# Optimization experiments

Measured on AMD Instinct MI355X. Metric: run time of the kernel, lower is better.

Reference implementation:

```python
import jax, jax.numpy as jnp
import numpy as np

TAU = 0.7
N_NODES = 1024
N_EDGES = 32768

def _mlp3(x, W1, b1, W2, b2, W3, b3):
    h = jax.nn.relu(x @ W1 + b1)
    h = jax.nn.relu(h @ W2 + b2)
    return h @ W3 + b3

def _gcn_conv(x, src, dst, W, b, n):
    # PyG GCNConv(add_self_loops=False): out = D^-1/2 A D^-1/2 (x W) + b
    deg = jax.ops.segment_sum(jnp.ones(src.shape[0], x.dtype), dst, num_segments=n)
    dinv = jnp.where(deg > 0, jax.lax.rsqrt(jnp.maximum(deg, 1.0)), 0.0)
    h = x @ W
    msg = h[src] * (dinv[src] * dinv[dst])[:, None]
    return jax.ops.segment_sum(msg, dst, num_segments=n) + b

def _forward(x1, x11, x2, mlp_W1, mlp_b1, mlp_W2, mlp_b2, mlp_W3, mlp_b3,
             m1_W1, m1_b1, m1_W2, m1_b2, m1_W3, m1_b3,
             wm1, bp1, bp2, wm12, wm13, class2,
             gcn1_W, gcn1_b, wm2, gcn2_W, gcn2_b, fc_W, fc_b, src, dst):
    n = x1.shape[0]
    logits = _mlp3(x1, mlp_W1, mlp_b1, mlp_W2, mlp_b2, mlp_W3, mlp_b3)  # [N,3]
    g = _mlp3(x11, m1_W1, m1_b1, m1_W2, m1_b2, m1_W3, m1_b3)            # [N,2]
    # hard argmax routing, softened: tau at argmax, (1-tau)/2 at the 2 others
    oh = jax.nn.one_hot(jnp.argmax(logits, axis=1), 3, dtype=logits.dtype)
    r = oh * TAU + (1.0 - oh) * ((1.0 - TAU) * 0.5)                     # [N,3]
    # fused form of: (einsum('nj,jkl',g,class2) * x2[...,None]).sum(-1) + g@b1
    res1 = jnp.einsum('nj,jkl,nk->nk', g, class2, x2) + g @ bp1         # [N,768]
    # fused form of: (einsum('nj,jkl',r,wm1) * res1[...,None]).sum(-1) + r@b2
    res1 = jnp.einsum('nj,jkl,nk->nk', r, wm1, res1) + r @ bp2          # [N,768]
    h1 = jax.nn.relu(_gcn_conv(res1, src, dst, gcn1_W, gcn1_b, n))      # [N,256]
    h1 = (r @ wm12) * h1 + 2e-4 * (res1 @ wm13)                         # [N,256]
    res2 = jnp.einsum('nj,jkl,nk->nk', r, wm2, h1)                      # [N,256]
    h2 = jax.nn.relu(_gcn_conv(res2, src, dst, gcn2_W, gcn2_b, n))      # [N,32]
    return jax.nn.log_softmax(h2 @ fc_W + fc_b, axis=1)                 # [N,8]

def setup_inputs():
    key = jax.random.key(0)
    ks = jax.random.split(key, 32)
    f = jnp.float32
    nrm = lambda i, s, sc=0.05: sc * jax.random.normal(ks[i], s, f)
    return {
        'x1': nrm(0, (N_NODES, 768), 1.0),
        'x11': nrm(1, (N_NODES, 768), 1.0),
        'x2': nrm(2, (N_NODES, 768), 1.0),
        'mlp_W1': nrm(3, (768, 512)), 'mlp_b1': jnp.zeros((512,), f),
        'mlp_W2': nrm(4, (512, 512)), 'mlp_b2': jnp.zeros((512,), f),
        'mlp_W3': nrm(5, (512, 3)), 'mlp_b3': jnp.zeros((3,), f),
        'm1_W1': nrm(6, (768, 512)), 'm1_b1': jnp.zeros((512,), f),
        'm1_W2': nrm(7, (512, 512)), 'm1_b2': jnp.zeros((512,), f),
        'm1_W3': nrm(8, (512, 2)), 'm1_b3': jnp.zeros((2,), f),
        'wm1': nrm(9, (3, 768, 256)),
        'bp1': jnp.zeros((2, 768), f),
        'bp2': jnp.zeros((3, 768), f),
        'wm12': jnp.ones((3, 256), f),
        'wm13': nrm(10, (768, 256)),
        'class2': jnp.ones((2, 768, 64), f),
        'gcn1_W': nrm(11, (768, 256)), 'gcn1_b': jnp.zeros((256,), f),
        'wm2': nrm(12, (3, 256, 256)),
        'gcn2_W': nrm(13, (256, 32)), 'gcn2_b': jnp.zeros((32,), f),
        'fc_W': nrm(14, (32, 8)), 'fc_b': jnp.zeros((8,), f),
        'edge_index': jax.random.randint(ks[15], (2, N_EDGES), 0, N_NODES),
    }

def reference(x1, x11, x2, mlp_W1, mlp_b1, mlp_W2, mlp_b2, mlp_W3, mlp_b3,
              m1_W1, m1_b1, m1_W2, m1_b2, m1_W3, m1_b3,
              wm1, bp1, bp2, wm12, wm13, class2,
              gcn1_W, gcn1_b, wm2, gcn2_W, gcn2_b, fc_W, fc_b, edge_index):
    src, dst = edge_index[0], edge_index[1]
    return _forward(x1, x11, x2, mlp_W1, mlp_b1, mlp_W2, mlp_b2, mlp_W3, mlp_b3,
                    m1_W1, m1_b1, m1_W2, m1_b2, m1_W3, m1_b3,
                    wm1, bp1, bp2, wm12, wm13, class2,
                    gcn1_W, gcn1_b, wm2, gcn2_W, gcn2_b, fc_W, fc_b, src, dst)
```

## Files before the change

kernel.cpp:

```cpp
#include <hip/hip_runtime.h>
#include <hip/hip_bf16.h>

#define NN 1024
#define NE 32768
#define TAU 0.7f
#define GAPT 0.01f

typedef __attribute__((ext_vector_type(8))) short short8;
typedef __attribute__((ext_vector_type(4))) float f32x4;

__device__ inline ushort bf16rne(float x) {
    union { float f; unsigned u; } a; a.f = x;
    unsigned r = (a.u + 0x7FFFu + ((a.u >> 16) & 1u)) >> 16;
    return (ushort)r;
}
__device__ inline float bf16tof(ushort h) {
    union { unsigned u; float f; } a; a.u = ((unsigned)h) << 16;
    return a.f;
}
__device__ inline void bf16split(float x, ushort& h, ushort& l) {
    h = bf16rne(x);
    l = bf16rne(x - bf16tof(h));
}

template <int K, int EPI>
__device__ __forceinline__ void gemm_wave(
    int lane, int rt, int ct,
    const ushort* __restrict__ Ah, const ushort* __restrict__ Al,
    const ushort* __restrict__ Bh, const ushort* __restrict__ Bl,
    const float* __restrict__ bias, const float* __restrict__ W3,
    float* __restrict__ Cf, ushort* __restrict__ Oh, ushort* __restrict__ Ol, int N) {
    int r0 = rt * 16, c0 = ct * 32;
    int g = lane >> 4, q = lane & 15;
    const ushort* pah = Ah + (size_t)(r0 + q) * K + g * 8;
    const ushort* pal = Al + (size_t)(r0 + q) * K + g * 8;
    const ushort* pb0h = Bh + (size_t)(c0 + q) * K + g * 8;
    const ushort* pb0l = Bl + (size_t)(c0 + q) * K + g * 8;
    const ushort* pb1h = pb0h + (size_t)16 * K;
    const ushort* pb1l = pb0l + (size_t)16 * K;
    f32x4 acc0 = {0.f, 0.f, 0.f, 0.f};
    f32x4 acc1 = {0.f, 0.f, 0.f, 0.f};
#pragma unroll 2
    for (int k0 = 0; k0 < K; k0 += 32) {
        short8 ah = *(const short8*)(pah + k0);
        short8 al = *(const short8*)(pal + k0);
        short8 b0h = *(const short8*)(pb0h + k0);
        short8 b0l = *(const short8*)(pb0l + k0);
        short8 b1h = *(const short8*)(pb1h + k0);
        short8 b1l = *(const short8*)(pb1l + k0);
        acc0 = __builtin_amdgcn_mfma_f32_16x16x32_bf16(ah, b0h, acc0, 0, 0, 0);
        acc1 = __builtin_amdgcn_mfma_f32_16x16x32_bf16(ah, b1h, acc1, 0, 0, 0);
        acc0 = __builtin_amdgcn_mfma_f32_16x16x32_bf16(ah, b0l, acc0, 0, 0, 0);
        acc1 = __builtin_amdgcn_mfma_f32_16x16x32_bf16(ah, b1l, acc1, 0, 0, 0);
        acc0 = __builtin_amdgcn_mfma_f32_16x16x32_bf16(al, b0h, acc0, 0, 0, 0);
        acc1 = __builtin_amdgcn_mfma_f32_16x16x32_bf16(al, b1h, acc1, 0, 0, 0);
    }
    int col0 = c0 + q, col1 = c0 + 16 + q;
    if constexpr (EPI == 0) {
#pragma unroll
        for (int i = 0; i < 4; i++) {
            int row = r0 + g * 4 + i;
            Cf[(size_t)row * N + col0] = acc0[i];
            Cf[(size_t)row * N + col1] = acc1[i];
        }
    } else if constexpr (EPI == 1) {
        float bv0 = bias[col0], bv1 = bias[col1];
#pragma unroll
        for (int i = 0; i < 4; i++) {
            int row = r0 + g * 4 + i;
            float a0 = fmaxf(acc0[i] + bv0, 0.f);
            float a1 = fmaxf(acc1[i] + bv1, 0.f);
            ushort h, l;
            bf16split(a0, h, l);
            Oh[(size_t)row * N + col0] = h;
            Ol[(size_t)row * N + col0] = l;
            bf16split(a1, h, l);
            Oh[(size_t)row * N + col1] = h;
            Ol[(size_t)row * N + col1] = l;
        }
    } else {
        constexpr int J = (EPI == 2) ? 3 : 2;
        constexpr int STR = (EPI == 2) ? 4 : 2;
        float bv0 = bias[col0], bv1 = bias[col1];
        float s[4][J];
#pragma unroll
        for (int i = 0; i < 4; i++) {
            float a0 = fmaxf(acc0[i] + bv0, 0.f);
            float a1 = fmaxf(acc1[i] + bv1, 0.f);
#pragma unroll
            for (int j = 0; j < J; j++)
                s[i][j] = a0 * W3[col0 * J + j] + a1 * W3[col1 * J + j];
        }
#pragma unroll
        for (int i = 0; i < 4; i++)
#pragma unroll
            for (int j = 0; j < J; j++) {
                float v = s[i][j];
#pragma unroll
                for (int m = 1; m < 16; m <<= 1) v += __shfl_xor(v, m);
                s[i][j] = v;
            }
        if (q == 0) {
#pragma unroll
            for (int i = 0; i < 4; i++) {
                int row = r0 + g * 4 + i;
#pragma unroll
                for (int j = 0; j < J; j++) atomicAdd(&Cf[(size_t)row * STR + j], s[i][j]);
            }
        }
    }
}

template <int M, int N, int K, int EPI>
__global__ __launch_bounds__(256) void gemm3(
    const ushort* __restrict__ Ah, const ushort* __restrict__ Al,
    const ushort* __restrict__ Bh, const ushort* __restrict__ Bl,
    float* __restrict__ Cf) {
    constexpr int RT = M / 16;
    constexpr int JOBS = RT * (N / 32);
    int wid = (blockIdx.x * 256 + threadIdx.x) >> 6;
    if (wid >= JOBS) return;
    gemm_wave<K, EPI>(threadIdx.x & 63, wid % RT, wid / RT, Ah, Al, Bh, Bl,
                      nullptr, nullptr, Cf, nullptr, nullptr, N);
}

template <int K, int EPI0, int EPI1, bool FILL>
__global__ __launch_bounds__(256) void gemm_pair(
    const ushort* __restrict__ Ah0, const ushort* __restrict__ Al0,
    const ushort* __restrict__ Bh0, const ushort* __restrict__ Bl0,
    const float* __restrict__ bias0, const float* __restrict__ W30,
    float* __restrict__ Cf0, ushort* __restrict__ Oh0, ushort* __restrict__ Ol0,
    const ushort* __restrict__ Ah1, const ushort* __restrict__ Al1,
    const ushort* __restrict__ Bh1, const ushort* __restrict__ Bl1,
    const float* __restrict__ bias1, const float* __restrict__ W31,
    float* __restrict__ Cf1, ushort* __restrict__ Oh1, ushort* __restrict__ Ol1,
    const int* __restrict__ esrc, const int* __restrict__ edst,
    int* __restrict__ cursor, int* __restrict__ adj) {
    if (FILL && blockIdx.x >= 512) {
        int e = (blockIdx.x - 512) * 256 + threadIdx.x;
        int d = edst[e];
        int slot = atomicAdd(&cursor[d], 1);
        adj[slot] = esrc[e];
        return;
    }
    int wid = (blockIdx.x * 256 + threadIdx.x) >> 6;
    int lane = threadIdx.x & 63;
    int pair = wid >> 10;
    int widl = wid & 1023;
    int rt = widl & 63, ct = widl >> 6;
    if (pair == 0)
        gemm_wave<K, EPI0>(lane, rt, ct, Ah0, Al0, Bh0, Bl0, bias0, W30, Cf0, Oh0, Ol0, 512);
    else
        gemm_wave<K, EPI1>(lane, rt, ct, Ah1, Al1, Bh1, Bl1, bias1, W31, Cf1, Oh1, Ol1, 512);
}

__device__ void dev_zero(int sub, int t, float* zbase) {
    for (int i = sub * 256 + t; i < 6144; i += 512) zbase[i] = 0.f;
}

__device__ void dev_tabs(int sub, int t, const float* class2, const float* wm1,
                         const float* wm2, float* C2s, float* Wm1s, float* Wm2s) {
    int i = sub * 256 + t;
    if (i < 1536) {
        const float* p = class2 + (size_t)i * 64;
        float s = 0.f;
        for (int l = 0; l < 64; l++) s += p[l];
        C2s[i] = s;
    } else if (i < 3840) {
        int j = i - 1536;
        const float* p = wm1 + (size_t)j * 256;
        float s = 0.f;
        for (int l = 0; l < 256; l++) s += p[l];
        Wm1s[j] = s;
    } else if (i < 4608) {
        int j = i - 3840;
        const float* p = wm2 + (size_t)j * 256;
        float s = 0.f;
        for (int l = 0; l < 256; l++) s += p[l];
        Wm2s[j] = s;
    }
}

__device__ void dev_splitx(int sub, int t, const float* __restrict__ X,
                           ushort* __restrict__ Xh, ushort* __restrict__ Xl) {
    int j = sub * 256 + t;
    float4 v = ((const float4*)X)[j];
    ushort h0, l0, h1, l1, h2, l2, h3, l3;
    bf16split(v.x, h0, l0);
    bf16split(v.y, h1, l1);
    bf16split(v.z, h2, l2);
    bf16split(v.w, h3, l3);
    ((ushort4*)Xh)[j] = make_ushort4(h0, h1, h2, h3);
    ((ushort4*)Xl)[j] = make_ushort4(l0, l1, l2, l3);
}

__device__ void dev_csr(int t, const int* __restrict__ edst, int* __restrict__ rowst,
                        int* __restrict__ cursor, float* __restrict__ dinv) {
    __shared__ int s[NN];
    s[t] = 0;
    __syncthreads();
    for (int j = 0; j < 32; j++) atomicAdd(&s[edst[j * 1024 + t]], 1);
    __syncthreads();
    int d = s[t];
    dinv[t] = d > 0 ? rsqrtf((float)d) : 0.f;
    __syncthreads();
    for (int off = 1; off < NN; off <<= 1) {
        int v = (t >= off) ? s[t - off] : 0;
        __syncthreads();
        s[t] += v;
        __syncthreads();
    }
    rowst[t + 1] = s[t];
    if (t == 0) rowst[0] = 0;
    cursor[t] = s[t] - d;
}

__global__ __launch_bounds__(1024) void aux0(
    const float* class2, const float* wm1, const float* wm2,
    float* C2s, float* Wm1s, float* Wm2s, float* zbase,
    const float* x1, ushort* XH1, ushort* XL1,
    const float* x11, ushort* XH2, ushort* XL2,
    const float* W1a, ushort* W1AH, ushort* W1AL,
    const float* W1b, ushort* W1BH, ushort* W1BL,
    const float* W2a, ushort* W2AH, ushort* W2AL,
    const float* W2b, ushort* W2BH, ushort* W2BL,
    const float* G1W, ushort* GWH, ushort* GWL,
    const float* W13, const float* G2W, ushort* G2TH, ushort* G2TL,
    const int* edst, int* rowst, int* cursor, float* dinv) {
    if (blockIdx.x == 807) {
        dev_csr(threadIdx.x, edst, rowst, cursor, dinv);
        return;
    }
    __shared__ float tb[4][32][33];
    int quad = threadIdx.x >> 8;
    int t = threadIdx.x & 255;
    int sub = blockIdx.x * 4 + quad;
    const float* W = nullptr;
    ushort *Th = nullptr, *Tl = nullptr;
    int K = 0, N = 0, tile = 0;
    if (sub >= 3220)      { W = G2W; Th = G2TH; Tl = G2TL; K = 256; N = 32;  tile = sub - 3220; }
    else if (sub >= 3028) { W = W13; Th = GWH + 256 * 768; Tl = GWL + 256 * 768; K = 768; N = 256; tile = sub - 3028; }
    else if (sub >= 2836) { W = G1W; Th = GWH; Tl = GWL; K = 768; N = 256; tile = sub - 2836; }
    else if (sub >= 2580) { W = W2b; Th = W2BH; Tl = W2BL; K = 512; N = 512; tile = sub - 2580; }
    else if (sub >= 2324) { W = W2a; Th = W2AH; Tl = W2AL; K = 512; N = 512; tile = sub - 2324; }
    else if (sub >= 1940) { W = W1b; Th = W1BH; Tl = W1BL; K = 768; N = 512; tile = sub - 1940; }
    else if (sub >= 1556) { W = W1a; Th = W1AH; Tl = W1AL; K = 768; N = 512; tile = sub - 1556; }
    int k0 = 0, n0 = 0;
    if (W) {
        k0 = (tile % (K / 32)) * 32;
        n0 = (tile / (K / 32)) * 32;
        int tx = t % 32, ty = t / 32;
        for (int i = ty; i < 32; i += 8)
            tb[quad][i][tx] = W[(size_t)(k0 + i) * N + n0 + tx];
    } else if (sub < 2) dev_zero(sub, t, zbase);
    else if (sub < 20) dev_tabs(sub - 2, t, class2, wm1, wm2, C2s, Wm1s, Wm2s);
    else if (sub < 788) dev_splitx(sub - 20, t, x1, XH1, XL1);
    else dev_splitx(sub - 788, t, x11, XH2, XL2);
    __syncthreads();
    if (W) {
        int tx = t % 32, ty = t / 32;
        for (int i = ty; i < 32; i += 8) {
            float v = tb[quad][tx][i];
            ushort h, l;
            bf16split(v, h, l);
            Th[(size_t)(n0 + i) * K + k0 + tx] = h;
            Tl[(size_t)(n0 + i) * K + k0 + tx] = l;
        }
    }
}

__global__ __launch_bounds__(256) void finrep(
    const float* __restrict__ LG, const float* __restrict__ b3, float* __restrict__ rbuf,
    const float* __restrict__ x1, const float* __restrict__ W1, const float* __restrict__ b1,
    const float* __restrict__ W2, const float* __restrict__ b2, const float* __restrict__ W3) {
    __shared__ int snode[4];
    __shared__ int scnt;
    __shared__ float part[4][512];
    __shared__ float xs[768];
    __shared__ float h1[512];
    __shared__ float h2[512];
    int t = threadIdx.x;
    if (t == 0) scnt = 0;
    __syncthreads();
    if (t < 4) {
        int n = blockIdx.x * 4 + t;
        float l0 = LG[n * 4 + 0] + b3[0];
        float l1 = LG[n * 4 + 1] + b3[1];
        float l2 = LG[n * 4 + 2] + b3[2];
        int am = 0;
        float mv = l0;
        if (l1 > mv) { mv = l1; am = 1; }
        if (l2 > mv) { mv = l2; am = 2; }
        float sec = (am == 0) ? fmaxf(l1, l2) : ((am == 1) ? fmaxf(l0, l2) : fmaxf(l0, l1));
        float lo = (1.f - TAU) * 0.5f;
        rbuf[n * 4 + 0] = (am == 0) ? TAU : lo;
        rbuf[n * 4 + 1] = (am == 1) ? TAU : lo;
        rbuf[n * 4 + 2] = (am == 2) ? TAU : lo;
        if (mv - sec < GAPT) {
            int s = atomicAdd(&scnt, 1);
            snode[s] = n;
        }
    }
    __syncthreads();
    int cnt = scnt;
    int w = t >> 6, l = t & 63;
    for (int it = 0; it < cnt; it++) {
        int n = snode[it];
        for (int k = t; k < 768; k += 256) xs[k] = x1[(size_t)n * 768 + k];
        __syncthreads();
        {
            float acc[8] = {0.f, 0.f, 0.f, 0.f, 0.f, 0.f, 0.f, 0.f};
            for (int k = w * 192; k < (w + 1) * 192; k++) {
                float xv = xs[k];
                const float* wr = W1 + (size_t)k * 512 + l;
#pragma unroll
                for (int c = 0; c < 8; c++) acc[c] += xv * wr[64 * c];
            }
#pragma unroll
            for (int c = 0; c < 8; c++) part[w][l + 64 * c] = acc[c];
        }
        __syncthreads();
        for (int d = t; d < 512; d += 256)
            h1[d] = fmaxf(part[0][d] + part[1][d] + part[2][d] + part[3][d] + b1[d], 0.f);
        __syncthreads();
        {
            float acc[8] = {0.f, 0.f, 0.f, 0.f, 0.f, 0.f, 0.f, 0.f};
            for (int k = w * 128; k < (w + 1) * 128; k++) {
                float xv = h1[k];
                const float* wr = W2 + (size_t)k * 512 + l;
#pragma unroll
                for (int c = 0; c < 8; c++) acc[c] += xv * wr[64 * c];
            }
#pragma unroll
            for (int c = 0; c < 8; c++) part[w][l + 64 * c] = acc[c];
        }
        __syncthreads();
        for (int d = t; d < 512; d += 256)
            h2[d] = fmaxf(part[0][d] + part[1][d] + part[2][d] + part[3][d] + b2[d], 0.f);
        __syncthreads();
        if (t < 64) {
            float p0 = 0.f, p1 = 0.f, p2 = 0.f;
            for (int k = t; k < 512; k += 64) {
                float hv = h2[k];
                p0 += hv * W3[k * 3 + 0];
                p1 += hv * W3[k * 3 + 1];
                p2 += hv * W3[k * 3 + 2];
            }
            for (int off = 32; off; off >>= 1) {
                p0 += __shfl_down(p0, off);
                p1 += __shfl_down(p1, off);
                p2 += __shfl_down(p2, off);
            }
            if (t == 0) {
                float l0 = p0 + b3[0], l1 = p1 + b3[1], l2 = p2 + b3[2];
                int am = 0;
                float mv = l0;
                if (l1 > mv) { mv = l1; am = 1; }
                if (l2 > mv) { mv = l2; am = 2; }
                float lo = (1.f - TAU) * 0.5f;
                rbuf[n * 4 + 0] = (am == 0) ? TAU : lo;
                rbuf[n * 4 + 1] = (am == 1) ? TAU : lo;
                rbuf[n * 4 + 2] = (am == 2) ? TAU : lo;
            }
        }
        __syncthreads();
    }
}

__global__ __launch_bounds__(256) void res1_kernel(
    const float* __restrict__ x2, const float* __restrict__ G, const float* __restrict__ m1b3,
    const float* __restrict__ rbuf, const float* __restrict__ C2s, const float* __restrict__ bp1,
    const float* __restrict__ Wm1s, const float* __restrict__ bp2,
    ushort* __restrict__ r1h, ushort* __restrict__ r1l) {
    int idx = blockIdx.x * 256 + threadIdx.x;
    int n = idx / 192;
    int kq = (idx % 192) * 4;
    float g0 = G[n * 2 + 0] + m1b3[0], g1 = G[n * 2 + 1] + m1b3[1];
    float r0 = rbuf[n * 4 + 0], r1 = rbuf[n * 4 + 1], r2 = rbuf[n * 4 + 2];
    float4 xv = *(const float4*)(x2 + (size_t)n * 768 + kq);
    float4 c0 = *(const float4*)(C2s + kq);
    float4 c1 = *(const float4*)(C2s + 768 + kq);
    float4 p0 = *(const float4*)(bp1 + kq);
    float4 p1 = *(const float4*)(bp1 + 768 + kq);
    float4 w0 = *(const float4*)(Wm1s + kq);
    float4 w1 = *(const float4*)(Wm1s + 768 + kq);
    float4 w2 = *(const float4*)(Wm1s + 1536 + kq);
    float4 q0 = *(const float4*)(bp2 + kq);
    float4 q1 = *(const float4*)(bp2 + 768 + kq);
    float4 q2 = *(const float4*)(bp2 + 1536 + kq);
    float o[4];
    o[0] = (xv.x * (g0 * c0.x + g1 * c1.x) + g0 * p0.x + g1 * p1.x) * (r0 * w0.x + r1 * w1.x + r2 * w2.x) + r0 * q0.x + r1 * q1.x + r2 * q2.x;
    o[1] = (xv.y * (g0 * c0.y + g1 * c1.y) + g0 * p0.y + g1 * p1.y) * (r0 * w0.y + r1 * w1.y + r2 * w2.y) + r0 * q0.y + r1 * q1.y + r2 * q2.y;
    o[2] = (xv.z * (g0 * c0.z + g1 * c1.z) + g0 * p0.z + g1 * p1.z) * (r0 * w0.z + r1 * w1.z + r2 * w2.z) + r0 * q0.z + r1 * q1.z + r2 * q2.z;
    o[3] = (xv.w * (g0 * c0.w + g1 * c1.w) + g0 * p0.w + g1 * p1.w) * (r0 * w0.w + r1 * w1.w + r2 * w2.w) + r0 * q0.w + r1 * q1.w + r2 * q2.w;
    ushort h[4], l[4];
#pragma unroll
    for (int i = 0; i < 4; i++) bf16split(o[i], h[i], l[i]);
    size_t off = ((size_t)n * 768 + kq) / 4;
    ((ushort4*)r1h)[off] = make_ushort4(h[0], h[1], h[2], h[3]);
    ((ushort4*)r1l)[off] = make_ushort4(l[0], l[1], l[2], l[3]);
}

__global__ __launch_bounds__(256) void gather1_combine(
    const float* __restrict__ gcw, const int* __restrict__ rowst, const int* __restrict__ adj,
    const float* __restrict__ dinv, const float* __restrict__ gcn1_b,
    const float* __restrict__ rbuf, const float* __restrict__ wm12,
    const float* __restrict__ Wm2s, ushort* __restrict__ res2h, ushort* __restrict__ res2l) {
    int n = blockIdx.x;
    int k = threadIdx.x;
    int lane = threadIdx.x & 63;
    int e0 = rowst[n], e1 = rowst[n + 1];
    float acc = 0.f;
    for (int base = e0; base < e1; base += 64) {
        int idx = base + lane;
        int s_i = 0;
        float w_i = 0.f;
        if (idx < e1) { s_i = adj[idx]; w_i = dinv[s_i]; }
        int mm = min(64, e1 - base);
        for (int j = 0; j < mm; j++) {
            int s = __shfl(s_i, j);
            float w = __shfl(w_i, j);
            acc += gcw[(size_t)s * 512 + k] * w;
        }
    }
    float h1 = dinv[n] * acc + gcn1_b[k];
    float mv = gcw[(size_t)n * 512 + 256 + k];
    float r0 = rbuf[n * 4 + 0], r1 = rbuf[n * 4 + 1], r2 = rbuf[n * 4 + 2];
    float a = r0 * wm12[k] + r1 * wm12[256 + k] + r2 * wm12[512 + k];
    float w = r0 * Wm2s[k] + r1 * Wm2s[256 + k] + r2 * Wm2s[512 + k];
    float v = w * (a * fmaxf(h1, 0.f) + 2e-4f * mv);
    ushort h, l;
    bf16split(v, h, l);
    res2h[(size_t)n * 256 + k] = h;
    res2l[(size_t)n * 256 + k] = l;
}

__global__ __launch_bounds__(64) void gather2_fc(
    const float* __restrict__ g2h, const int* __restrict__ rowst, const int* __restrict__ adj,
    const float* __restrict__ dinv, const float* __restrict__ gcn2_b,
    const float* __restrict__ fcW, const float* __restrict__ fcb, float* __restrict__ out) {
    __shared__ float h2s[2][32];
    int t = threadIdx.x;
    int half = t >> 5, k = t & 31;
    int n = blockIdx.x * 2 + half;
    int e0 = rowst[n], e1 = rowst[n + 1];
    float acc = 0.f;
    for (int base = e0; base < e1; base += 32) {
        int idx = base + k;
        int s_i = 0;
        float w_i = 0.f;
        if (idx < e1) { s_i = adj[idx]; w_i = dinv[s_i]; }
        int mm = min(32, e1 - base);
        for (int j = 0; j < mm; j++) {
            int s = __shfl(s_i, j, 32);
            float w = __shfl(w_i, j, 32);
            acc += g2h[(size_t)s * 32 + k] * w;
        }
    }
    h2s[half][k] = fmaxf(dinv[n] * acc + gcn2_b[k], 0.f);
    __syncthreads();
    if (t < 16) {
        int nn = t >> 3, j = t & 7;
        const float* hr = h2s[nn];
        float logit = fcb[j];
#pragma unroll
        for (int i = 0; i < 32; i++) logit += hr[i] * fcW[i * 8 + j];
        float m = logit;
        for (int off = 4; off; off >>= 1) m = fmaxf(m, __shfl_xor(m, off, 8));
        float e = expf(logit - m), s = e;
        for (int off = 4; off; off >>= 1) s += __shfl_xor(s, off, 8);
        out[(size_t)(blockIdx.x * 2 + nn) * 8 + j] = logit - m - logf(s);
    }
}

extern "C" void kernel_launch(void* const* d_in, const int* in_sizes, int n_in,
                              void* d_out, int out_size, void* d_ws, size_t ws_size,
                              hipStream_t stream) {
    const float* x1     = (const float*)d_in[0];
    const float* x11    = (const float*)d_in[1];
    const float* x2     = (const float*)d_in[2];
    const float* mlp_W1 = (const float*)d_in[3];
    const float* mlp_b1 = (const float*)d_in[4];
    const float* mlp_W2 = (const float*)d_in[5];
    const float* mlp_b2 = (const float*)d_in[6];
    const float* mlp_W3 = (const float*)d_in[7];
    const float* mlp_b3 = (const float*)d_in[8];
    const float* m1_W1  = (const float*)d_in[9];
    const float* m1_b1  = (const float*)d_in[10];
    const float* m1_W2  = (const float*)d_in[11];
    const float* m1_b2  = (const float*)d_in[12];
    const float* m1_W3  = (const float*)d_in[13];
    const float* m1_b3  = (const float*)d_in[14];
    const float* wm1    = (const float*)d_in[15];
    const float* bp1    = (const float*)d_in[16];
    const float* bp2    = (const float*)d_in[17];
    const float* wm12   = (const float*)d_in[18];
    const float* wm13   = (const float*)d_in[19];
    const float* class2 = (const float*)d_in[20];
    const float* gcn1_W = (const float*)d_in[21];
    const float* gcn1_b = (const float*)d_in[22];
    const float* wm2    = (const float*)d_in[23];
    const float* gcn2_W = (const float*)d_in[24];
    const float* gcn2_b = (const float*)d_in[25];
    const float* fc_W   = (const float*)d_in[26];
    const float* fc_b   = (const float*)d_in[27];
    const int* eidx     = (const int*)d_in[28];
    const int* esrc = eidx;
    const int* edst = eidx + NE;

    char* ws = (char*)d_ws;
    ushort* XH1   = (ushort*)(ws + 0x0000000);
    ushort* XL1   = (ushort*)(ws + 0x0180000);
    ushort* XH2   = (ushort*)(ws + 0x0300000);
    ushort* XL2   = (ushort*)(ws + 0x0480000);
    ushort* W1AH  = (ushort*)(ws + 0x0600000);
    ushort* W1AL  = (ushort*)(ws + 0x06C0000);
    ushort* W1BH  = (ushort*)(ws + 0x0780000);
    ushort* W1BL  = (ushort*)(ws + 0x0840000);
    ushort* W2AH  = (ushort*)(ws + 0x0900000);
    ushort* W2AL  = (ushort*)(ws + 0x0980000);
    ushort* W2BH  = (ushort*)(ws + 0x0A00000);
    ushort* W2BL  = (ushort*)(ws + 0x0A80000);
    ushort* GWH   = (ushort*)(ws + 0x0B00000);
    ushort* GWL   = (ushort*)(ws + 0x0BC0000);
    ushort* G2TH  = (ushort*)(ws + 0x0C80000);
    ushort* G2TL  = (ushort*)(ws + 0x0C84000);
    ushort* HS1AH = (ushort*)(ws + 0x0D00000);
    ushort* HS1AL = (ushort*)(ws + 0x0E00000);
    ushort* HS1BH = (ushort*)(ws + 0x0F00000);
    ushort* HS1BL = (ushort*)(ws + 0x1000000);
    ushort* RES1H = (ushort*)(ws + 0x1100000);
    ushort* RES1L = (ushort*)(ws + 0x1280000);
    float*  GCW   = (float*)(ws + 0x1400000);
    ushort* RES2H = (ushort*)(ws + 0x1600000);
    ushort* RES2L = (ushort*)(ws + 0x1680000);
    float*  G2H   = (float*)(ws + 0x1700000);
    float* LOGITS = (float*)(ws + 0x1740000);
    float* GBUF   = (float*)(ws + 0x1744000);
    float* RBUF   = (float*)(ws + 0x1746000);
    float* DINV   = (float*)(ws + 0x174A000);
    int*   ROWST  = (int*)(ws + 0x174B000);
    int*   CURS   = (int*)(ws + 0x174D000);
    int*   ADJ    = (int*)(ws + 0x174E000);
    float* C2S    = (float*)(ws + 0x1770000);
    float* WM1S   = (float*)(ws + 0x1772000);
    float* WM2S   = (float*)(ws + 0x1775000);

    aux0<<<808, 1024, 0, stream>>>(class2, wm1, wm2, C2S, WM1S, WM2S, LOGITS,
                                   x1, XH1, XL1, x11, XH2, XL2,
                                   mlp_W1, W1AH, W1AL, m1_W1, W1BH, W1BL,
                                   mlp_W2, W2AH, W2AL, m1_W2, W2BH, W2BL,
                                   gcn1_W, GWH, GWL, wm13, gcn2_W, G2TH, G2TL,
                                   edst, ROWST, CURS, DINV);
    gemm_pair<768, 1, 1, true><<<640, 256, 0, stream>>>(
        XH1, XL1, W1AH, W1AL, mlp_b1, nullptr, nullptr, HS1AH, HS1AL,
        XH2, XL2, W1BH, W1BL, m1_b1, nullptr, nullptr, HS1BH, HS1BL,
        esrc, edst, CURS, ADJ);
    gemm_pair<512, 2, 3, false><<<512, 256, 0, stream>>>(
        HS1AH, HS1AL, W2AH, W2AL, mlp_b2, mlp_W3, LOGITS, nullptr, nullptr,
        HS1BH, HS1BL, W2BH, W2BL, m1_b2, m1_W3, GBUF, nullptr, nullptr,
        nullptr, nullptr, nullptr, nullptr);
    finrep<<<256, 256, 0, stream>>>(LOGITS, mlp_b3, RBUF, x1, mlp_W1, mlp_b1,
                                    mlp_W2, mlp_b2, mlp_W3);
    res1_kernel<<<768, 256, 0, stream>>>(x2, GBUF, m1_b3, RBUF, C2S, bp1, WM1S, bp2,
                                         RES1H, RES1L);
    gemm3<1024, 512, 768, 0><<<256, 256, 0, stream>>>(RES1H, RES1L, GWH, GWL, GCW);
    gather1_combine<<<NN, 256, 0, stream>>>(GCW, ROWST, ADJ, DINV, gcn1_b, RBUF,
                                            wm12, WM2S, RES2H, RES2L);
    gemm3<1024, 32, 256, 0><<<16, 256, 0, stream>>>(RES2H, RES2L, G2TH, G2TL, G2H);
    gather2_fc<<<NN / 2, 64, 0, stream>>>(G2H, ROWST, ADJ, DINV, gcn2_b, fc_W, fc_b,
                                          (float*)d_out);
}
```

Baseline: 193.3 us.

## Split CSR build across kernels: parallel degree count, scan rider, fill rider

```diff
diff --git a/kernel.cpp b/kernel.cpp
--- a/kernel.cpp
+++ b/kernel.cpp
@@ -124,7 +124,7 @@
                       nullptr, nullptr, Cf, nullptr, nullptr, N);
 }
 
-template <int K, int EPI0, int EPI1, bool FILL>
+template <int K, int EPI0, int EPI1, int RIDER>
 __global__ __launch_bounds__(256) void gemm_pair(
     const ushort* __restrict__ Ah0, const ushort* __restrict__ Al0,
     const ushort* __restrict__ Bh0, const ushort* __restrict__ Bl0,
@@ -135,8 +135,39 @@
     const float* __restrict__ bias1, const float* __restrict__ W31,
     float* __restrict__ Cf1, ushort* __restrict__ Oh1, ushort* __restrict__ Ol1,
     const int* __restrict__ esrc, const int* __restrict__ edst,
-    int* __restrict__ cursor, int* __restrict__ adj) {
-    if (FILL && blockIdx.x >= 512) {
+    const int* __restrict__ deg, int* __restrict__ rowst, int* __restrict__ cursor,
+    float* __restrict__ dinv, int* __restrict__ adj) {
+    if (RIDER == 1 && blockIdx.x >= 512) {
+        __shared__ int ps[256];
+        int t = threadIdx.x;
+        int4 d4 = *(const int4*)(deg + t * 4);
+        int sum = d4.x + d4.y + d4.z + d4.w;
+        ps[t] = sum;
+        __syncthreads();
+        for (int off = 1; off < 256; off <<= 1) {
+            int v = (t >= off) ? ps[t - off] : 0;
+            __syncthreads();
+            ps[t] += v;
+            __syncthreads();
+        }
+        int r0 = ps[t] - sum;
+        int r1 = r0 + d4.x, r2 = r1 + d4.y, r3 = r2 + d4.z;
+        rowst[t * 4 + 0] = r0;
+        rowst[t * 4 + 1] = r1;
+        rowst[t * 4 + 2] = r2;
+        rowst[t * 4 + 3] = r3;
+        if (t == 255) rowst[1024] = r3 + d4.w;
+        cursor[t * 4 + 0] = r0;
+        cursor[t * 4 + 1] = r1;
+        cursor[t * 4 + 2] = r2;
+        cursor[t * 4 + 3] = r3;
+        dinv[t * 4 + 0] = d4.x > 0 ? rsqrtf((float)d4.x) : 0.f;
+        dinv[t * 4 + 1] = d4.y > 0 ? rsqrtf((float)d4.y) : 0.f;
+        dinv[t * 4 + 2] = d4.z > 0 ? rsqrtf((float)d4.z) : 0.f;
+        dinv[t * 4 + 3] = d4.w > 0 ? rsqrtf((float)d4.w) : 0.f;
+        return;
+    }
+    if (RIDER == 2 && blockIdx.x >= 512) {
         int e = (blockIdx.x - 512) * 256 + threadIdx.x;
         int d = edst[e];
         int slot = atomicAdd(&cursor[d], 1);
@@ -194,27 +225,6 @@
     ((ushort4*)Xl)[j] = make_ushort4(l0, l1, l2, l3);
 }
 
-__device__ void dev_csr(int t, const int* __restrict__ edst, int* __restrict__ rowst,
-                        int* __restrict__ cursor, float* __restrict__ dinv) {
-    __shared__ int s[NN];
-    s[t] = 0;
-    __syncthreads();
-    for (int j = 0; j < 32; j++) atomicAdd(&s[edst[j * 1024 + t]], 1);
-    __syncthreads();
-    int d = s[t];
-    dinv[t] = d > 0 ? rsqrtf((float)d) : 0.f;
-    __syncthreads();
-    for (int off = 1; off < NN; off <<= 1) {
-        int v = (t >= off) ? s[t - off] : 0;
-        __syncthreads();
-        s[t] += v;
-        __syncthreads();
-    }
-    rowst[t + 1] = s[t];
-    if (t == 0) rowst[0] = 0;
-    cursor[t] = s[t] - d;
-}
-
 __global__ __launch_bounds__(1024) void aux0(
     const float* class2, const float* wm1, const float* wm2,
     float* C2s, float* Wm1s, float* Wm2s, float* zbase,
@@ -226,11 +236,7 @@
     const float* W2b, ushort* W2BH, ushort* W2BL,
     const float* G1W, ushort* GWH, ushort* GWL,
     const float* W13, const float* G2W, ushort* G2TH, ushort* G2TL,
-    const int* edst, int* rowst, int* cursor, float* dinv) {
-    if (blockIdx.x == 807) {
-        dev_csr(threadIdx.x, edst, rowst, cursor, dinv);
-        return;
-    }
+    const int* edst, int* deg) {
     __shared__ float tb[4][32][33];
     int quad = threadIdx.x >> 8;
     int t = threadIdx.x & 255;
@@ -238,7 +244,11 @@
     const float* W = nullptr;
     ushort *Th = nullptr, *Tl = nullptr;
     int K = 0, N = 0, tile = 0;
-    if (sub >= 3220)      { W = G2W; Th = G2TH; Tl = G2TL; K = 256; N = 32;  tile = sub - 3220; }
+    if (sub >= 3228) {
+        int e = (sub - 3228) * 256 + t;
+        atomicAdd(&deg[edst[e]], 1);
+    }
+    else if (sub >= 3220) { W = G2W; Th = G2TH; Tl = G2TL; K = 256; N = 32;  tile = sub - 3220; }
     else if (sub >= 3028) { W = W13; Th = GWH + 256 * 768; Tl = GWL + 256 * 768; K = 768; N = 256; tile = sub - 3028; }
     else if (sub >= 2836) { W = G1W; Th = GWH; Tl = GWL; K = 768; N = 256; tile = sub - 2836; }
     else if (sub >= 2580) { W = W2b; Th = W2BH; Tl = W2BL; K = 512; N = 512; tile = sub - 2580; }
@@ -255,7 +265,7 @@
     } else if (sub < 2) dev_zero(sub, t, zbase);
     else if (sub < 20) dev_tabs(sub - 2, t, class2, wm1, wm2, C2s, Wm1s, Wm2s);
     else if (sub < 788) dev_splitx(sub - 20, t, x1, XH1, XL1);
-    else dev_splitx(sub - 788, t, x11, XH2, XL2);
+    else if (sub < 1556) dev_splitx(sub - 788, t, x11, XH2, XL2);
     __syncthreads();
     if (W) {
         int tx = t % 32, ty = t / 32;
@@ -542,24 +552,26 @@
     int*   ROWST  = (int*)(ws + 0x174B000);
     int*   CURS   = (int*)(ws + 0x174D000);
     int*   ADJ    = (int*)(ws + 0x174E000);
+    int*   DEG    = (int*)(ws + 0x176E000);
     float* C2S    = (float*)(ws + 0x1770000);
     float* WM1S   = (float*)(ws + 0x1772000);
     float* WM2S   = (float*)(ws + 0x1775000);
 
-    aux0<<<808, 1024, 0, stream>>>(class2, wm1, wm2, C2S, WM1S, WM2S, LOGITS,
+    hipMemsetAsync(DEG, 0, NN * sizeof(int), stream);
+    aux0<<<839, 1024, 0, stream>>>(class2, wm1, wm2, C2S, WM1S, WM2S, LOGITS,
                                    x1, XH1, XL1, x11, XH2, XL2,
                                    mlp_W1, W1AH, W1AL, m1_W1, W1BH, W1BL,
                                    mlp_W2, W2AH, W2AL, m1_W2, W2BH, W2BL,
                                    gcn1_W, GWH, GWL, wm13, gcn2_W, G2TH, G2TL,
-                                   edst, ROWST, CURS, DINV);
-    gemm_pair<768, 1, 1, true><<<640, 256, 0, stream>>>(
+                                   edst, DEG);
+    gemm_pair<768, 1, 1, 1><<<513, 256, 0, stream>>>(
         XH1, XL1, W1AH, W1AL, mlp_b1, nullptr, nullptr, HS1AH, HS1AL,
         XH2, XL2, W1BH, W1BL, m1_b1, nullptr, nullptr, HS1BH, HS1BL,
-        esrc, edst, CURS, ADJ);
-    gemm_pair<512, 2, 3, false><<<512, 256, 0, stream>>>(
+        esrc, edst, DEG, ROWST, CURS, DINV, ADJ);
+    gemm_pair<512, 2, 3, 2><<<640, 256, 0, stream>>>(
         HS1AH, HS1AL, W2AH, W2AL, mlp_b2, mlp_W3, LOGITS, nullptr, nullptr,
         HS1BH, HS1BL, W2BH, W2BL, m1_b2, m1_W3, GBUF, nullptr, nullptr,
-        nullptr, nullptr, nullptr, nullptr);
+        esrc, edst, DEG, ROWST, CURS, DINV, ADJ);
     finrep<<<256, 256, 0, stream>>>(LOGITS, mlp_b3, RBUF, x1, mlp_W1, mlp_b1,
                                     mlp_W2, mlp_b2, mlp_W3);
     res1_kernel<<<768, 256, 0, stream>>>(x2, GBUF, m1_b3, RBUF, C2S, bp1, WM1S, bp2,
```

After: 202.9 us. 5.0% more time.
